# Kernel optimization log

Hardware: AMD Instinct MI355X
Metric: run time of the kernel (lower is better)

Reference implementation:

```python
import jax, jax.numpy as jnp
import numpy as np
from jax import lax

S_DET, S_ANG = 725, 360   # detector bins, projection angles
OUT = 512                 # reconstructed image side
NNZ = 8388608             # nonzeros in sparse backprojection matrix AT
BATCH = 4
BN_EPS = 1e-3             # keras BatchNormalization default epsilon


def _ramp_filter():
    # w_bfunction(pi, linspace(-362, 362, 725))
    s = np.linspace(-np.floor(S_DET / 2), S_DET - np.floor(S_DET / 2) - 1, S_DET)
    v = np.pi * s
    u = np.empty_like(v)
    z = v == 0
    u[z] = 0.5
    nz = ~z
    u[nz] = (np.cos(v[nz]) - 1.0) / v[nz] ** 2 + np.sin(v[nz]) / v[nz]
    return (u * np.pi ** 2 / (4.0 * np.pi ** 2)).astype(np.float32)


def setup_inputs() -> dict:
    key = jax.random.key(0)
    ks = jax.random.split(key, 24)
    p = 0.05
    inp = {
        'inputs': jax.random.normal(ks[0], (BATCH, S_DET, S_ANG, 1), jnp.float32),
        'w_sin1': jax.random.normal(ks[1], (5, 5, 1, 64), jnp.float32) * p,
        'b_sin1': jnp.zeros((64,), jnp.float32),
        'w_sin_mid': jax.random.normal(ks[2], (4, 5, 5, 64, 64), jnp.float32) * p,
        'sin_gamma': jnp.ones((4, 64), jnp.float32),
        'sin_beta': jnp.zeros((4, 64), jnp.float32),
        'sin_mean': jax.random.normal(ks[3], (4, 64), jnp.float32) * 0.1,
        'sin_var': jax.random.uniform(ks[4], (4, 64), jnp.float32, 0.5, 1.5),
        'w_sin6': jax.random.normal(ks[5], (5, 5, 64, 1), jnp.float32) * p,
        'b_sin6': jnp.zeros((1,), jnp.float32),
        'w_ct1': jax.random.normal(ks[6], (5, 5, 1, 64), jnp.float32) * p,
        'b_ct1': jnp.zeros((64,), jnp.float32),
        'w_ct_mid': jax.random.normal(ks[7], (5, 5, 5, 64, 64), jnp.float32) * p,
        'ct_gamma': jnp.ones((5, 64), jnp.float32),
        'ct_beta': jnp.zeros((5, 64), jnp.float32),
        'ct_mean': jax.random.normal(ks[8], (5, 64), jnp.float32) * 0.1,
        'ct_var': jax.random.uniform(ks[9], (5, 64), jnp.float32, 0.5, 1.5),
        'w_ct6': jax.random.normal(ks[10], (5, 5, 64, 1), jnp.float32) * p,
        'b_ct6': jnp.zeros((1,), jnp.float32),
        'w_b': jnp.asarray(_ramp_filter()),
        'at_vals': jax.random.uniform(ks[11], (NNZ,), jnp.float32) * 1e-3,
        'at_rows': jnp.sort(jax.random.randint(ks[12], (NNZ,), 0, OUT * OUT, jnp.int32)),
        'at_cols': jax.random.randint(ks[13], (NNZ,), 0, S_DET * S_ANG, jnp.int32),
    }
    return inp


def _conv2d(x, w, b=None):
    y = lax.conv_general_dilated(x, w, (1, 1), 'SAME',
                                 dimension_numbers=('NHWC', 'HWIO', 'NHWC'))
    return y if b is None else y + b


def _bn(x, g, b, m, v):
    return (x - m) * (g * lax.rsqrt(v + BN_EPS)) + b


def _decode(sin_fan, w_b, at_vals, at_rows, at_cols):
    B = sin_fan.shape[0]
    sf = jnp.transpose(sin_fan, (0, 2, 1, 3))          # [B, 360, 725, 1]
    x = sf.reshape(-1, S_DET, 1)                       # [B*360, 725, 1]
    k = w_b.reshape(S_DET, 1, 1)
    f = lax.conv_general_dilated(x, k, (1,), 'SAME',
                                 dimension_numbers=('NWC', 'WIO', 'NWC'))
    f2 = f.reshape(B, -1).T                            # [261000, B]
    # sparse AT @ f2 via gather + segment_sum
    contrib = at_vals[:, None] * f2[at_cols]           # [nnz, B]
    rf = jax.ops.segment_sum(contrib, at_rows, num_segments=OUT * OUT)
    return 4.0 * rf.T.reshape(B, OUT, OUT, 1)


def reference(inputs, w_sin1, b_sin1, w_sin_mid, sin_gamma, sin_beta, sin_mean,
              sin_var, w_sin6, b_sin6, w_ct1, b_ct1, w_ct_mid, ct_gamma,
              ct_beta, ct_mean, ct_var, w_ct6, b_ct6, w_b, at_vals,
              at_rows, at_cols):
    # --- sinogram domain residual CNN ---
    de = jax.nn.relu(_conv2d(inputs, w_sin1, b_sin1))
    pp = de
    for i in range(4):  # M1 residual blocks
        de = jax.nn.relu(_bn(_conv2d(de, w_sin_mid[i]), sin_gamma[i],
                             sin_beta[i], sin_mean[i], sin_var[i]))
        pp = de + pp
    de_sin = _conv2d(pp / 4.0, w_sin6, b_sin6) + inputs
    # --- filtered backprojection ---
    fbp = _decode(de_sin, w_b, at_vals, at_rows, at_cols)
    # --- image domain residual CNN ---
    out = jax.nn.relu(_conv2d(fbp, w_ct1, b_ct1))
    qq = out
    for i in range(5):  # M2 residual blocks
        out = jax.nn.relu(_bn(_conv2d(out, w_ct_mid[i]), ct_gamma[i],
                              ct_beta[i], ct_mean[i], ct_var[i]))
        qq = qq + out
    outputs = _conv2d(qq / 5.0, w_ct6, b_ct6) + fbp
    return (de_sin, outputs, fbp)
```

## Files before the change

kernel.cpp:

```cpp
#include <hip/hip_runtime.h>
#include <stdint.h>

#define S_DET 725
#define S_ANG 360
#define OUTD  512
#define NB    4

typedef float    float4v __attribute__((ext_vector_type(4)));
typedef int      int4v   __attribute__((ext_vector_type(4)));
typedef _Float16 half8   __attribute__((ext_vector_type(8)));
typedef _Float16 half4   __attribute__((ext_vector_type(4)));
typedef _Float16 half2v  __attribute__((ext_vector_type(2)));

#define GAS __attribute__((address_space(1)))
#define LAS __attribute__((address_space(3)))

__device__ __forceinline__ void async16(const void* src, void* lds) {
  __builtin_amdgcn_global_load_lds((const GAS void*)(uintptr_t)src,
                                   (LAS void*)(uint32_t)(uintptr_t)lds, 16, 0, 0);
}

__global__ __launch_bounds__(256)
void prep_weights(const float* __restrict__ wsin, const float* __restrict__ sg,
                  const float* __restrict__ sb,  const float* __restrict__ sm,
                  const float* __restrict__ sv,
                  const float* __restrict__ wct, const float* __restrict__ cg,
                  const float* __restrict__ cbt, const float* __restrict__ cm,
                  const float* __restrict__ cv,
                  const float* __restrict__ wsin6, const float* __restrict__ wct6,
                  _Float16* __restrict__ wout, float* __restrict__ bout,
                  _Float16* __restrict__ w6out)
{
  int id = blockIdx.x * 256 + threadIdx.x;
  if (id < 9 * 102400) {
    int l   = id / 102400;
    int rem = id - l * 102400;
    int t = rem >> 12;
    int kn = rem & 4095;
    int k = kn >> 6, n = kn & 63;
    const float *w, *g, *b, *m, *v;
    if (l < 4) { w = wsin + l*102400; g = sg + l*64; b = sb + l*64; m = sm + l*64; v = sv + l*64; }
    else { int li = l - 4; w = wct + li*102400; g = cg + li*64; b = cbt + li*64; m = cm + li*64; v = cv + li*64; }
    float s = g[n] * rsqrtf(v[n] + 1e-3f);
    float val = w[rem] * s;
    int slot = (k >> 3) ^ (n & 7);
    wout[(size_t)l*102400 + t*4096 + n*64 + slot*8 + (k & 7)] = (_Float16)val;
    if (rem < 64)
      bout[l*64 + rem] = b[rem] - m[rem] * s;
  } else {
    int r = id - 9 * 102400;
    if (r < 3200)
      w6out[r] = (_Float16)(r < 1600 ? wsin6[r] : wct6[r - 1600]);
  }
}

template <int IMG>
__global__ __launch_bounds__(256)
void conv1_kernel(const float* __restrict__ src, _Float16* __restrict__ dst,
                  const float* __restrict__ w1, const float* __restrict__ b1,
                  int H, int W, int b0)
{
  __shared__ __align__(16) float in_s[400];
  __shared__ __align__(16) float w_s[1600];
  __shared__ float b_s[64];
  const int tid = threadIdx.x;
  const int bz = blockIdx.z, gb = b0 + bz;
  const int y0 = blockIdx.y * 16, x0 = blockIdx.x * 16;
  for (int i = tid; i < 1600; i += 256) w_s[i] = w1[i];
  if (tid < 64) b_s[tid] = b1[tid];
  for (int i = tid; i < 400; i += 256) {
    int iy = i / 20, ix = i - iy * 20;
    int y = y0 - 2 + iy, x = x0 - 2 + ix;
    float v = 0.f;
    if (y >= 0 && y < H && x >= 0 && x < W) {
      if (IMG) v = 4.f * src[(size_t)(y * W + x) * 4 + gb];
      else     v = src[((size_t)gb * H + y) * W + x];
    }
    in_s[i] = v;
  }
  __syncthreads();
  const int ty = tid >> 4, tx = tid & 15;
  float acc[64];
#pragma unroll
  for (int c = 0; c < 64; ++c) acc[c] = 0.f;
  int dy = 0, dx = 0;
  for (int t = 0; t < 25; ++t) {
    float v = in_s[(ty + dy) * 20 + tx + dx];
    const float4v* wp = (const float4v*)(w_s + t * 64);
#pragma unroll
    for (int c = 0; c < 16; ++c) {
      float4v w4 = wp[c];
      acc[4*c+0] += v * w4[0]; acc[4*c+1] += v * w4[1];
      acc[4*c+2] += v * w4[2]; acc[4*c+3] += v * w4[3];
    }
    if (++dx == 5) { dx = 0; ++dy; }
  }
  const int y = y0 + ty, x = x0 + tx;
  if (y < H && x < W) {
    uint32_t* dp = (uint32_t*)(dst + ((size_t)(bz * H + y) * W + x) * 64);
#pragma unroll
    for (int c = 0; c < 32; ++c) {
      float v0 = acc[2*c]   + b_s[2*c];   v0 = v0 > 0.f ? v0 : 0.f;
      float v1 = acc[2*c+1] + b_s[2*c+1]; v1 = v1 > 0.f ? v1 : 0.f;
      half2v h = { (_Float16)v0, (_Float16)v1 };
      dp[c] = __builtin_bit_cast(uint32_t, h);
    }
  }
}

__global__ __launch_bounds__(256, 2)
void mid_conv(const _Float16* __restrict__ src, _Float16* __restrict__ dst,
              float* __restrict__ accum,
              const _Float16* __restrict__ wt, const _Float16* __restrict__ w6g,
              const float* __restrict__ bias, const char* __restrict__ zbuf,
              int H, int W, int b0)
{
  __shared__ __align__(16) char smem[51200 + 2 * 8192 + 3200 + 16];
  char* const atile = smem;
  char* const wbuf  = smem + 51200;
  _Float16* const w6l = (_Float16*)(smem + 51200 + 16384);
  char* const zl = smem + 51200 + 16384 + 3200;
  const int tid = threadIdx.x;
  const int wv = tid >> 6, ln = tid & 63;
  const int bz = blockIdx.z, gb = b0 + bz;
  const int y0 = blockIdx.y * 16, x0 = blockIdx.x * 16;

  if (tid < 200) ((half8*)w6l)[tid] = ((const half8*)w6g)[tid];
  if (tid < 4) ((int*)zl)[tid] = 0;

  for (int inst = wv; inst < 50; inst += 4) {
    const int slot = inst * 64 + ln;
    const int p = slot >> 3, gp = slot & 7;
    const int g = gp ^ (p & 7);
    const int iy = p / 20, ix = p - iy * 20;
    const int y = y0 - 2 + iy, x = x0 - 2 + ix;
    const char* sp = (y >= 0 && y < H && x >= 0 && x < W)
        ? (const char*)(src + ((size_t)(bz * H + y) * W + x) * 64) + g * 16
        : zbuf + g * 16;
    async16(sp, atile + inst * 1024);
  }
#pragma unroll
  for (int j = 0; j < 2; ++j) {
    const int inst = wv * 2 + j;
    async16((const char*)wt + inst * 1024 + ln * 16, wbuf + inst * 1024);
  }
  __syncthreads();

  float4v acc[4][4];
  float4v acc6[4];
#pragma unroll
  for (int pi = 0; pi < 4; ++pi) {
    acc6[pi] = (float4v){0.f, 0.f, 0.f, 0.f};
#pragma unroll
    for (int ci = 0; ci < 4; ++ci) acc[pi][ci] = (float4v){0.f, 0.f, 0.f, 0.f};
  }

  int dy = 0, dx = 0;
  for (int t = 0; t < 25; ++t) {
    if (t < 24) {
      char* wdst = wbuf + ((t + 1) & 1) * 8192;
#pragma unroll
      for (int j = 0; j < 2; ++j) {
        const int inst = wv * 2 + j;
        async16((const char*)wt + (t + 1) * 8192 + inst * 1024 + ln * 16,
                wdst + inst * 1024);
      }
    }
    const char* wb = wbuf + (t & 1) * 8192;
#pragma unroll
    for (int kc = 0; kc < 2; ++kc) {
      const int g0 = kc * 4 + (ln >> 4);
      half8 wf[4], af[4], wf6;
#pragma unroll
      for (int ci = 0; ci < 4; ++ci) {
        const int ch = ci * 16 + (ln & 15);
        wf[ci] = *(const half8*)(wb + ch * 128 + ((g0 ^ (ch & 7)) << 4));
      }
      wf6 = *(const half8*)((ln & 15) == 0
                ? (const char*)(w6l + t * 64 + kc * 32 + ((ln >> 4) << 3))
                : zl);
#pragma unroll
      for (int pi = 0; pi < 4; ++pi) {
        const int p = (wv * 4 + pi + dy) * 20 + (ln & 15) + dx;
        af[pi] = *(const half8*)(atile + p * 128 + ((g0 ^ (p & 7)) << 4));
      }
#pragma unroll
      for (int pi = 0; pi < 4; ++pi) {
#pragma unroll
        for (int ci = 0; ci < 4; ++ci)
          acc[pi][ci] = __builtin_amdgcn_mfma_f32_16x16x32_f16(
              wf[ci], af[pi], acc[pi][ci], 0, 0, 0);
        acc6[pi] = __builtin_amdgcn_mfma_f32_16x16x32_f16(
            wf6, af[pi], acc6[pi], 0, 0, 0);
      }
    }
    if (++dx == 5) { dx = 0; ++dy; }
    __syncthreads();
  }

  const int tx = ln & 15;
  const int x = x0 + tx;
#pragma unroll
  for (int pi = 0; pi < 4; ++pi) {
    const int y = y0 + wv * 4 + pi;
    if (y < H && x < W) {
      _Float16* dp = dst + ((size_t)(bz * H + y) * W + x) * 64;
#pragma unroll
      for (int ci = 0; ci < 4; ++ci) {
        const int cbase = ci * 16 + (ln >> 4) * 4;
        const float4v bv = *(const float4v*)(bias + cbase);
        half4 h;
#pragma unroll
        for (int r = 0; r < 4; ++r) {
          float v = acc[pi][ci][r] + bv[r];
          v = v > 0.f ? v : 0.f;
          h[r] = (_Float16)v;
        }
        *(half4*)(dp + cbase) = h;
      }
    }
  }
  if (ln < 16) {
#pragma unroll
    for (int pi = 0; pi < 4; ++pi) {
      const int y = y0 + wv * 4 + pi, x2 = x0 + ln;
      if (y < H && x2 < W)
        accum[((size_t)gb * H + y) * W + x2] += acc6[pi][0];
    }
  }
}

__global__ __launch_bounds__(256, 2)
void fc_accum(const _Float16* __restrict__ src, float* __restrict__ accum,
              const float* __restrict__ w6, const char* __restrict__ zbuf,
              int H, int W, int b0)
{
  __shared__ __align__(16) char smem[51200 + 3200];
  char* const atile = smem;
  _Float16* const wl = (_Float16*)(smem + 51200);
  const int tid = threadIdx.x;
  const int wv = tid >> 6, ln = tid & 63;
  const int bz = blockIdx.z, gb = b0 + bz;
  const int y0 = blockIdx.y * 16, x0 = blockIdx.x * 16;
  for (int i = tid; i < 1600; i += 256) wl[i] = (_Float16)w6[i];
  for (int inst = wv; inst < 50; inst += 4) {
    const int slot = inst * 64 + ln;
    const int p = slot >> 3, gp = slot & 7;
    const int g = gp ^ (p & 7);
    const int iy = p / 20, ix = p - iy * 20;
    const int y = y0 - 2 + iy, x = x0 - 2 + ix;
    const char* sp = (y >= 0 && y < H && x >= 0 && x < W)
        ? (const char*)(src + ((size_t)(bz * H + y) * W + x) * 64) + g * 16
        : zbuf + g * 16;
    async16(sp, atile + inst * 1024);
  }
  __syncthreads();
  const int ty = tid >> 4, tx = tid & 15;
  float sum = 0.f;
  int dy = 0, dxx = 0;
  for (int t = 0; t < 25; ++t) {
    const int p = (ty + dy) * 20 + tx + dxx;
    const char* pb = atile + p * 128;
    const int pk = p & 7;
    const half2v* wp = (const half2v*)(wl + t * 64);
#pragma unroll
    for (int g = 0; g < 8; ++g) {
      half8 h = *(const half8*)(pb + ((g ^ pk) << 4));
#pragma unroll
      for (int q = 0; q < 4; ++q) {
        half2v a = { h[2*q], h[2*q+1] };
        sum = __builtin_amdgcn_fdot2(a, wp[g * 4 + q], sum, false);
      }
    }
    if (++dxx == 5) { dxx = 0; ++dy; }
  }
  const int y = y0 + ty, x = x0 + tx;
  if (y < H && x < W) accum[((size_t)gb * H + y) * W + x] += sum;
}

__global__ __launch_bounds__(256)
void write_desin(const float* __restrict__ accf, const float* __restrict__ inputs,
                 const float* __restrict__ b6, float* __restrict__ out)
{
  int id = blockIdx.x * 256 + threadIdx.x;
  if (id < NB * S_DET * S_ANG) out[id] = accf[id] * 0.25f + b6[0] + inputs[id];
}

__global__ __launch_bounds__(128)
void ramp_filter(const float* __restrict__ desin, const float* __restrict__ wb,
                 _Float16* __restrict__ f2h)
{
  __shared__ float col[1472];
  __shared__ float wl[725];
  const int blk = blockIdx.x;
  const int b = blk / 360, a = blk - b * 360;
  const int tid = threadIdx.x;
  for (int i = tid; i < 1472; i += 128) col[i] = 0.f;
  for (int i = tid; i < 725; i += 128) wl[i] = wb[i];
  __syncthreads();
  for (int i = tid; i < 725; i += 128) col[368 + i] = desin[(b * 725 + i) * 360 + a];
  __syncthreads();
  const int s0 = tid * 6;
  if (s0 < 725) {
    float o0 = 0, o1 = 0, o2 = 0, o3 = 0, o4 = 0, o5 = 0;
    const float* cb = col + 6 + s0;
    float r0 = cb[0], r1 = cb[1], r2 = cb[2], r3 = cb[3], r4 = cb[4], r5 = cb[5];
    for (int t = 0; t < 725; ++t) {
      float w = wl[t];
      o0 += r0 * w; o1 += r1 * w; o2 += r2 * w;
      o3 += r3 * w; o4 += r4 * w; o5 += r5 * w;
      r0 = r1; r1 = r2; r2 = r3; r3 = r4; r4 = r5; r5 = cb[t + 6];
    }
    float o[6] = { o0, o1, o2, o3, o4, o5 };
#pragma unroll
    for (int j = 0; j < 6; ++j)
      if (s0 + j < 725) f2h[((size_t)a * 725 + s0 + j) * 4 + b] = (_Float16)o[j];
  }
}

__global__ __launch_bounds__(256)
void backproj(const float* __restrict__ vals, const int* __restrict__ rows,
              const int* __restrict__ cols, const _Float16* __restrict__ f2h,
              float* __restrict__ rf)
{
  const int tid = blockIdx.x * 256 + threadIdx.x;
  const int i0 = tid * 16;
  const int4v* rp = (const int4v*)(rows + i0);
  const int4v* cp = (const int4v*)(cols + i0);
  const float4v* vp = (const float4v*)(vals + i0);
  float a0 = 0, a1 = 0, a2 = 0, a3 = 0;
  int4v r0v = __builtin_nontemporal_load(rp);
  int cur = r0v[0];
#pragma unroll
  for (int q = 0; q < 4; ++q) {
    int4v r4 = (q == 0) ? r0v : __builtin_nontemporal_load(rp + q);
    int4v c4 = __builtin_nontemporal_load(cp + q);
    float4v v4 = __builtin_nontemporal_load(vp + q);
#pragma unroll
    for (int u = 0; u < 4; ++u) {
      int r = r4[u]; int c = c4[u]; float v = v4[u];
      if (r != cur) {
        atomicAdd(rf + (size_t)cur * 4 + 0, a0);
        atomicAdd(rf + (size_t)cur * 4 + 1, a1);
        atomicAdd(rf + (size_t)cur * 4 + 2, a2);
        atomicAdd(rf + (size_t)cur * 4 + 3, a3);
        a0 = a1 = a2 = a3 = 0; cur = r;
      }
      const half4 f = *(const half4*)(f2h + (size_t)c * 4);
      a0 += v * (float)f[0]; a1 += v * (float)f[1];
      a2 += v * (float)f[2]; a3 += v * (float)f[3];
    }
  }
  atomicAdd(rf + (size_t)cur * 4 + 0, a0);
  atomicAdd(rf + (size_t)cur * 4 + 1, a1);
  atomicAdd(rf + (size_t)cur * 4 + 2, a2);
  atomicAdd(rf + (size_t)cur * 4 + 3, a3);
}

__global__ __launch_bounds__(256)
void write_fbp(const float* __restrict__ rf, float* __restrict__ out)
{
  int id = blockIdx.x * 256 + threadIdx.x;
  int b = id >> 18, p = id & 262143;
  out[id] = 4.f * rf[(size_t)p * 4 + b];
}

__global__ __launch_bounds__(256)
void write_outputs(const float* __restrict__ accf, const float* __restrict__ rf,
                   const float* __restrict__ b6, float* __restrict__ out)
{
  int id = blockIdx.x * 256 + threadIdx.x;
  int b = id >> 18, p = id & 262143;
  out[id] = accf[id] * 0.2f + b6[0] + 4.f * rf[(size_t)p * 4 + b];
}

extern "C" void kernel_launch(void* const* d_in, const int* in_sizes, int n_in,
                              void* d_out, int out_size, void* d_ws, size_t ws_size,
                              hipStream_t stream)
{
  (void)in_sizes; (void)n_in; (void)out_size;
  const float* inputs   = (const float*)d_in[0];
  const float* w_sin1   = (const float*)d_in[1];
  const float* b_sin1   = (const float*)d_in[2];
  const float* w_sin_mid= (const float*)d_in[3];
  const float* sin_gamma= (const float*)d_in[4];
  const float* sin_beta = (const float*)d_in[5];
  const float* sin_mean = (const float*)d_in[6];
  const float* sin_var  = (const float*)d_in[7];
  const float* w_sin6   = (const float*)d_in[8];
  const float* b_sin6   = (const float*)d_in[9];
  const float* w_ct1    = (const float*)d_in[10];
  const float* b_ct1    = (const float*)d_in[11];
  const float* w_ct_mid = (const float*)d_in[12];
  const float* ct_gamma = (const float*)d_in[13];
  const float* ct_beta  = (const float*)d_in[14];
  const float* ct_mean  = (const float*)d_in[15];
  const float* ct_var   = (const float*)d_in[16];
  const float* w_ct6    = (const float*)d_in[17];
  const float* b_ct6    = (const float*)d_in[18];
  const float* w_b      = (const float*)d_in[19];
  const float* at_vals  = (const float*)d_in[20];
  const int*   at_rows  = (const int*)d_in[21];
  const int*   at_cols  = (const int*)d_in[22];
  float* out = (float*)d_out;

  const size_t base = (size_t)11 << 20;
  const size_t act_per_batch = (size_t)2 * 262144 * 128;
  int nbat = 1;
  if (ws_size >= base + 4 * act_per_batch) nbat = 4;
  else if (ws_size >= base + 2 * act_per_batch) nbat = 2;
  const int npass = 4 / nbat;

  char* ws = (char*)d_ws;
  size_t off = 0;
  auto alloc = [&](size_t bytes) {
    char* p = ws + off;
    off = (off + bytes + 255) & ~(size_t)255;
    return p;
  };
  char*     zbuf    = alloc(256);
  _Float16* wmid    = (_Float16*)alloc((size_t)9 * 102400 * 2);
  float*    biasmid = (float*)alloc(9 * 64 * 4);
  _Float16* w6s     = (_Float16*)alloc(3200 * 2);
  float*    rf      = (float*)alloc((size_t)262144 * 16);
  char*     shreg   = alloc((size_t)262144 * 16);
  _Float16* act_a   = (_Float16*)alloc((size_t)nbat * 262144 * 128);
  _Float16* act_b   = (_Float16*)alloc((size_t)nbat * 262144 * 128);
  _Float16* f2h    = (_Float16*)shreg;
  float*    acc_fc = (float*)shreg;

  hipMemsetAsync(zbuf, 0, 256, stream);
  hipMemsetAsync(rf, 0, (size_t)262144 * 16, stream);
  hipMemsetAsync(acc_fc, 0, (size_t)262144 * 16, stream);

  prep_weights<<<3613, 256, 0, stream>>>(w_sin_mid, sin_gamma, sin_beta, sin_mean, sin_var,
                                         w_ct_mid, ct_gamma, ct_beta, ct_mean, ct_var,
                                         w_sin6, w_ct6, wmid, biasmid, w6s);

  for (int p = 0; p < npass; ++p) {
    const int b0 = p * nbat;
    conv1_kernel<0><<<dim3(23, 46, nbat), 256, 0, stream>>>(inputs, act_a, w_sin1, b_sin1,
                                                            725, 360, b0);
    _Float16* cur = act_a; _Float16* nxt = act_b;
    for (int i = 0; i < 4; ++i) {
      mid_conv<<<dim3(23, 46, nbat), 256, 0, stream>>>(cur, nxt, acc_fc,
                                                       wmid + (size_t)i * 102400, w6s,
                                                       biasmid + i * 64, zbuf, 725, 360, b0);
      _Float16* t = cur; cur = nxt; nxt = t;
    }
    fc_accum<<<dim3(23, 46, nbat), 256, 0, stream>>>(cur, acc_fc, w_sin6, zbuf, 725, 360, b0);
  }
  write_desin<<<4079, 256, 0, stream>>>(acc_fc, inputs, b_sin6, out);

  ramp_filter<<<1440, 128, 0, stream>>>(out, w_b, f2h);
  backproj<<<2048, 256, 0, stream>>>(at_vals, at_rows, at_cols, f2h, rf);
  write_fbp<<<4096, 256, 0, stream>>>(rf, out + 2092576);

  hipMemsetAsync(acc_fc, 0, (size_t)262144 * 16, stream);
  for (int p = 0; p < npass; ++p) {
    const int b0 = p * nbat;
    conv1_kernel<1><<<dim3(32, 32, nbat), 256, 0, stream>>>(rf, act_a, w_ct1, b_ct1,
                                                            512, 512, b0);
    _Float16* cur = act_a; _Float16* nxt = act_b;
    for (int i = 0; i < 5; ++i) {
      mid_conv<<<dim3(32, 32, nbat), 256, 0, stream>>>(cur, nxt, acc_fc,
                                                       wmid + (size_t)(4 + i) * 102400,
                                                       w6s + 1600,
                                                       biasmid + (4 + i) * 64, zbuf,
                                                       512, 512, b0);
      _Float16* t = cur; cur = nxt; nxt = t;
    }
    fc_accum<<<dim3(32, 32, nbat), 256, 0, stream>>>(cur, acc_fc, w_ct6, zbuf, 512, 512, b0);
  }
  write_outputs<<<4096, 256, 0, stream>>>(acc_fc, rf, b_ct6, out + 1044000);
}
```

Baseline: 2.752 ms.

## Move conv1 and final 1-channel conv to MFMA, coarsen backprojection atomics

The first 1-to-64 convolution is rebuilt as an im2col tile in shared memory feeding MFMA, using pre-packed fp16 weights. The final 64-to-1 reduction kernel now uses MFMA with a zero-padded weight fragment, and mid_conv reads that fragment directly from global memory instead of staging it in shared memory. Backprojection threads now handle 64 nonzeros each and use plain stores for rows they fully own, keeping atomics only for the first and last rows. Together these aim to cut scalar FMA work, LDS use and atomic traffic, at the cost of fp16 rounding in conv1 and extra global weight loads.

```diff
diff --git a/kernel.cpp b/kernel.cpp
--- a/kernel.cpp
+++ b/kernel.cpp
@@ -28,8 +28,9 @@
                   const float* __restrict__ cbt, const float* __restrict__ cm,
                   const float* __restrict__ cv,
                   const float* __restrict__ wsin6, const float* __restrict__ wct6,
+                  const float* __restrict__ wsin1, const float* __restrict__ wct1,
                   _Float16* __restrict__ wout, float* __restrict__ bout,
-                  _Float16* __restrict__ w6out)
+                  _Float16* __restrict__ w6out, _Float16* __restrict__ w1fout)
 {
   int id = blockIdx.x * 256 + threadIdx.x;
   if (id < 9 * 102400) {
@@ -49,25 +50,34 @@
       bout[l*64 + rem] = b[rem] - m[rem] * s;
   } else {
     int r = id - 9 * 102400;
-    if (r < 3200)
+    if (r < 3200) {
       w6out[r] = (_Float16)(r < 1600 ? wsin6[r] : wct6[r - 1600]);
+    } else if (r < 3200 + 4096) {
+      int q = r - 3200;
+      int layer = q >> 11;
+      int idx = q & 2047;
+      int ci = idx >> 9, ln = (idx >> 3) & 63, e = idx & 7;
+      int ch = ci * 16 + (ln & 15);
+      int k = (ln >> 4) * 8 + e;
+      float val = 0.f;
+      if (k < 25) val = (layer ? wct1 : wsin1)[k * 64 + ch];
+      w1fout[q] = (_Float16)val;
+    }
   }
 }
 
 template <int IMG>
 __global__ __launch_bounds__(256)
-void conv1_kernel(const float* __restrict__ src, _Float16* __restrict__ dst,
-                  const float* __restrict__ w1, const float* __restrict__ b1,
-                  int H, int W, int b0)
-{
-  __shared__ __align__(16) float in_s[400];
-  __shared__ __align__(16) float w_s[1600];
-  __shared__ float b_s[64];
+void conv1_mfma(const float* __restrict__ src, _Float16* __restrict__ dst,
+                const _Float16* __restrict__ w1f, const float* __restrict__ b1,
+                int H, int W, int b0)
+{
+  __shared__ __align__(16) float rawt[400];
+  __shared__ __align__(16) char imc[256 * 80];
   const int tid = threadIdx.x;
+  const int wv = tid >> 6, ln = tid & 63;
   const int bz = blockIdx.z, gb = b0 + bz;
   const int y0 = blockIdx.y * 16, x0 = blockIdx.x * 16;
-  for (int i = tid; i < 1600; i += 256) w_s[i] = w1[i];
-  if (tid < 64) b_s[tid] = b1[tid];
   for (int i = tid; i < 400; i += 256) {
     int iy = i / 20, ix = i - iy * 20;
     int y = y0 - 2 + iy, x = x0 - 2 + ix;
@@ -76,34 +86,66 @@
       if (IMG) v = 4.f * src[(size_t)(y * W + x) * 4 + gb];
       else     v = src[((size_t)gb * H + y) * W + x];
     }
-    in_s[i] = v;
+    rawt[i] = v;
   }
   __syncthreads();
-  const int ty = tid >> 4, tx = tid & 15;
-  float acc[64];
-#pragma unroll
-  for (int c = 0; c < 64; ++c) acc[c] = 0.f;
-  int dy = 0, dx = 0;
-  for (int t = 0; t < 25; ++t) {
-    float v = in_s[(ty + dy) * 20 + tx + dx];
-    const float4v* wp = (const float4v*)(w_s + t * 64);
-#pragma unroll
-    for (int c = 0; c < 16; ++c) {
-      float4v w4 = wp[c];
-      acc[4*c+0] += v * w4[0]; acc[4*c+1] += v * w4[1];
-      acc[4*c+2] += v * w4[2]; acc[4*c+3] += v * w4[3];
-    }
-    if (++dx == 5) { dx = 0; ++dy; }
-  }
-  const int y = y0 + ty, x = x0 + tx;
-  if (y < H && x < W) {
-    uint32_t* dp = (uint32_t*)(dst + ((size_t)(bz * H + y) * W + x) * 64);
-#pragma unroll
-    for (int c = 0; c < 32; ++c) {
-      float v0 = acc[2*c]   + b_s[2*c];   v0 = v0 > 0.f ? v0 : 0.f;
-      float v1 = acc[2*c+1] + b_s[2*c+1]; v1 = v1 > 0.f ? v1 : 0.f;
-      half2v h = { (_Float16)v0, (_Float16)v1 };
-      dp[c] = __builtin_bit_cast(uint32_t, h);
+  {
+    const int ty = tid >> 4, tx = tid & 15;
+    _Float16 row[32];
+    int dy = 0, dx = 0;
+#pragma unroll
+    for (int t = 0; t < 25; ++t) {
+      row[t] = (_Float16)rawt[(ty + dy) * 20 + tx + dx];
+      if (++dx == 5) { dx = 0; ++dy; }
+    }
+#pragma unroll
+    for (int t = 25; t < 32; ++t) row[t] = (_Float16)0.f;
+    char* dp = imc + tid * 80;
+#pragma unroll
+    for (int j = 0; j < 4; ++j)
+      *(half8*)(dp + j * 16) = *(const half8*)((const char*)row + j * 16);
+  }
+  __syncthreads();
+
+  half8 wf[4];
+#pragma unroll
+  for (int ci = 0; ci < 4; ++ci) wf[ci] = ((const half8*)w1f)[ci * 64 + ln];
+
+  float4v acc[4][4];
+#pragma unroll
+  for (int pi = 0; pi < 4; ++pi)
+#pragma unroll
+    for (int ci = 0; ci < 4; ++ci) acc[pi][ci] = (float4v){0.f, 0.f, 0.f, 0.f};
+
+#pragma unroll
+  for (int pi = 0; pi < 4; ++pi) {
+    const int px = (wv * 4 + pi) * 16 + (ln & 15);
+    half8 af = *(const half8*)(imc + px * 80 + ((ln >> 4) << 4));
+#pragma unroll
+    for (int ci = 0; ci < 4; ++ci)
+      acc[pi][ci] = __builtin_amdgcn_mfma_f32_16x16x32_f16(wf[ci], af, acc[pi][ci], 0, 0, 0);
+  }
+
+  const int tx = ln & 15;
+  const int x = x0 + tx;
+#pragma unroll
+  for (int pi = 0; pi < 4; ++pi) {
+    const int y = y0 + wv * 4 + pi;
+    if (y < H && x < W) {
+      _Float16* dp = dst + ((size_t)(bz * H + y) * W + x) * 64;
+#pragma unroll
+      for (int ci = 0; ci < 4; ++ci) {
+        const int cbase = ci * 16 + (ln >> 4) * 4;
+        const float4v bv = *(const float4v*)(b1 + cbase);
+        half4 h;
+#pragma unroll
+        for (int r = 0; r < 4; ++r) {
+          float v = acc[pi][ci][r] + bv[r];
+          v = v > 0.f ? v : 0.f;
+          h[r] = (_Float16)v;
+        }
+        *(half4*)(dp + cbase) = h;
+      }
     }
   }
 }
@@ -115,18 +157,13 @@
               const float* __restrict__ bias, const char* __restrict__ zbuf,
               int H, int W, int b0)
 {
-  __shared__ __align__(16) char smem[51200 + 2 * 8192 + 3200 + 16];
+  __shared__ __align__(16) char smem[51200 + 2 * 8192];
   char* const atile = smem;
   char* const wbuf  = smem + 51200;
-  _Float16* const w6l = (_Float16*)(smem + 51200 + 16384);
-  char* const zl = smem + 51200 + 16384 + 3200;
   const int tid = threadIdx.x;
   const int wv = tid >> 6, ln = tid & 63;
   const int bz = blockIdx.z, gb = b0 + bz;
   const int y0 = blockIdx.y * 16, x0 = blockIdx.x * 16;
-
-  if (tid < 200) ((half8*)w6l)[tid] = ((const half8*)w6g)[tid];
-  if (tid < 4) ((int*)zl)[tid] = 0;
 
   for (int inst = wv; inst < 50; inst += 4) {
     const int slot = inst * 64 + ln;
@@ -170,15 +207,16 @@
 #pragma unroll
     for (int kc = 0; kc < 2; ++kc) {
       const int g0 = kc * 4 + (ln >> 4);
-      half8 wf[4], af[4], wf6;
+      half8 wf[4], af[4];
+      half8 wf6 = {(_Float16)0, (_Float16)0, (_Float16)0, (_Float16)0,
+                   (_Float16)0, (_Float16)0, (_Float16)0, (_Float16)0};
 #pragma unroll
       for (int ci = 0; ci < 4; ++ci) {
         const int ch = ci * 16 + (ln & 15);
         wf[ci] = *(const half8*)(wb + ch * 128 + ((g0 ^ (ch & 7)) << 4));
       }
-      wf6 = *(const half8*)((ln & 15) == 0
-                ? (const char*)(w6l + t * 64 + kc * 32 + ((ln >> 4) << 3))
-                : zl);
+      if ((ln & 15) == 0)
+        wf6 = *(const half8*)(w6g + t * 64 + kc * 32 + ((ln >> 4) << 3));
 #pragma unroll
       for (int pi = 0; pi < 4; ++pi) {
         const int p = (wv * 4 + pi + dy) * 20 + (ln & 15) + dx;
@@ -230,19 +268,16 @@
   }
 }
 
-__global__ __launch_bounds__(256, 2)
-void fc_accum(const _Float16* __restrict__ src, float* __restrict__ accum,
-              const float* __restrict__ w6, const char* __restrict__ zbuf,
-              int H, int W, int b0)
-{
-  __shared__ __align__(16) char smem[51200 + 3200];
-  char* const atile = smem;
-  _Float16* const wl = (_Float16*)(smem + 51200);
+__global__ __launch_bounds__(256, 3)
+void fc_mfma(const _Float16* __restrict__ src, float* __restrict__ accum,
+             const _Float16* __restrict__ w6g, const char* __restrict__ zbuf,
+             int H, int W, int b0)
+{
+  __shared__ __align__(16) char atile[51200];
   const int tid = threadIdx.x;
   const int wv = tid >> 6, ln = tid & 63;
   const int bz = blockIdx.z, gb = b0 + bz;
   const int y0 = blockIdx.y * 16, x0 = blockIdx.x * 16;
-  for (int i = tid; i < 1600; i += 256) wl[i] = (_Float16)w6[i];
   for (int inst = wv; inst < 50; inst += 4) {
     const int slot = inst * 64 + ln;
     const int p = slot >> 3, gp = slot & 7;
@@ -255,27 +290,37 @@
     async16(sp, atile + inst * 1024);
   }
   __syncthreads();
-  const int ty = tid >> 4, tx = tid & 15;
-  float sum = 0.f;
-  int dy = 0, dxx = 0;
+
+  float4v acc6[4];
+#pragma unroll
+  for (int pi = 0; pi < 4; ++pi) acc6[pi] = (float4v){0.f, 0.f, 0.f, 0.f};
+
+  int dy = 0, dx = 0;
   for (int t = 0; t < 25; ++t) {
-    const int p = (ty + dy) * 20 + tx + dxx;
-    const char* pb = atile + p * 128;
-    const int pk = p & 7;
-    const half2v* wp = (const half2v*)(wl + t * 64);
-#pragma unroll
-    for (int g = 0; g < 8; ++g) {
-      half8 h = *(const half8*)(pb + ((g ^ pk) << 4));
-#pragma unroll
-      for (int q = 0; q < 4; ++q) {
-        half2v a = { h[2*q], h[2*q+1] };
-        sum = __builtin_amdgcn_fdot2(a, wp[g * 4 + q], sum, false);
-      }
-    }
-    if (++dxx == 5) { dxx = 0; ++dy; }
-  }
-  const int y = y0 + ty, x = x0 + tx;
-  if (y < H && x < W) accum[((size_t)gb * H + y) * W + x] += sum;
+#pragma unroll
+    for (int kc = 0; kc < 2; ++kc) {
+      const int g0 = kc * 4 + (ln >> 4);
+      half8 wf6 = {(_Float16)0, (_Float16)0, (_Float16)0, (_Float16)0,
+                   (_Float16)0, (_Float16)0, (_Float16)0, (_Float16)0};
+      if ((ln & 15) == 0)
+        wf6 = *(const half8*)(w6g + t * 64 + kc * 32 + ((ln >> 4) << 3));
+#pragma unroll
+      for (int pi = 0; pi < 4; ++pi) {
+        const int p = (wv * 4 + pi + dy) * 20 + (ln & 15) + dx;
+        half8 af = *(const half8*)(atile + p * 128 + ((g0 ^ (p & 7)) << 4));
+        acc6[pi] = __builtin_amdgcn_mfma_f32_16x16x32_f16(wf6, af, acc6[pi], 0, 0, 0);
+      }
+    }
+    if (++dx == 5) { dx = 0; ++dy; }
+  }
+  if (ln < 16) {
+#pragma unroll
+    for (int pi = 0; pi < 4; ++pi) {
+      const int y = y0 + wv * 4 + pi, x2 = x0 + ln;
+      if (y < H && x2 < W)
+        accum[((size_t)gb * H + y) * W + x2] += acc6[pi][0];
+    }
+  }
 }
 
 __global__ __launch_bounds__(256)
@@ -324,15 +369,16 @@
               float* __restrict__ rf)
 {
   const int tid = blockIdx.x * 256 + threadIdx.x;
-  const int i0 = tid * 16;
+  const size_t i0 = (size_t)tid * 64;
   const int4v* rp = (const int4v*)(rows + i0);
   const int4v* cp = (const int4v*)(cols + i0);
   const float4v* vp = (const float4v*)(vals + i0);
   float a0 = 0, a1 = 0, a2 = 0, a3 = 0;
   int4v r0v = __builtin_nontemporal_load(rp);
   int cur = r0v[0];
-#pragma unroll
-  for (int q = 0; q < 4; ++q) {
+  bool first = true;
+#pragma unroll 4
+  for (int q = 0; q < 16; ++q) {
     int4v r4 = (q == 0) ? r0v : __builtin_nontemporal_load(rp + q);
     int4v c4 = __builtin_nontemporal_load(cp + q);
     float4v v4 = __builtin_nontemporal_load(vp + q);
@@ -340,10 +386,14 @@
     for (int u = 0; u < 4; ++u) {
       int r = r4[u]; int c = c4[u]; float v = v4[u];
       if (r != cur) {
-        atomicAdd(rf + (size_t)cur * 4 + 0, a0);
-        atomicAdd(rf + (size_t)cur * 4 + 1, a1);
-        atomicAdd(rf + (size_t)cur * 4 + 2, a2);
-        atomicAdd(rf + (size_t)cur * 4 + 3, a3);
+        float* p = rf + (size_t)cur * 4;
+        if (first) {
+          atomicAdd(p + 0, a0); atomicAdd(p + 1, a1);
+          atomicAdd(p + 2, a2); atomicAdd(p + 3, a3);
+          first = false;
+        } else {
+          p[0] = a0; p[1] = a1; p[2] = a2; p[3] = a3;
+        }
         a0 = a1 = a2 = a3 = 0; cur = r;
       }
       const half4 f = *(const half4*)(f2h + (size_t)c * 4);
@@ -351,10 +401,9 @@
       a2 += v * (float)f[2]; a3 += v * (float)f[3];
     }
   }
-  atomicAdd(rf + (size_t)cur * 4 + 0, a0);
-  atomicAdd(rf + (size_t)cur * 4 + 1, a1);
-  atomicAdd(rf + (size_t)cur * 4 + 2, a2);
-  atomicAdd(rf + (size_t)cur * 4 + 3, a3);
+  float* p = rf + (size_t)cur * 4;
+  atomicAdd(p + 0, a0); atomicAdd(p + 1, a1);
+  atomicAdd(p + 2, a2); atomicAdd(p + 3, a3);
 }
 
 __global__ __launch_bounds__(256)
@@ -422,6 +471,7 @@
   _Float16* wmid    = (_Float16*)alloc((size_t)9 * 102400 * 2);
   float*    biasmid = (float*)alloc(9 * 64 * 4);
   _Float16* w6s     = (_Float16*)alloc(3200 * 2);
+  _Float16* w1f     = (_Float16*)alloc(4096 * 2);
   float*    rf      = (float*)alloc((size_t)262144 * 16);
   char*     shreg   = alloc((size_t)262144 * 16);
   _Float16* act_a   = (_Float16*)alloc((size_t)nbat * 262144 * 128);
@@ -433,14 +483,15 @@
   hipMemsetAsync(rf, 0, (size_t)262144 * 16, stream);
   hipMemsetAsync(acc_fc, 0, (size_t)262144 * 16, stream);
 
-  prep_weights<<<3613, 256, 0, stream>>>(w_sin_mid, sin_gamma, sin_beta, sin_mean, sin_var,
+  prep_weights<<<3630, 256, 0, stream>>>(w_sin_mid, sin_gamma, sin_beta, sin_mean, sin_var,
                                          w_ct_mid, ct_gamma, ct_beta, ct_mean, ct_var,
-                                         w_sin6, w_ct6, wmid, biasmid, w6s);
+                                         w_sin6, w_ct6, w_sin1, w_ct1,
+                                         wmid, biasmid, w6s, w1f);
 
   for (int p = 0; p < npass; ++p) {
     const int b0 = p * nbat;
-    conv1_kernel<0><<<dim3(23, 46, nbat), 256, 0, stream>>>(inputs, act_a, w_sin1, b_sin1,
-                                                            725, 360, b0);
+    conv1_mfma<0><<<dim3(23, 46, nbat), 256, 0, stream>>>(inputs, act_a, w1f, b_sin1,
+                                                          725, 360, b0);
     _Float16* cur = act_a; _Float16* nxt = act_b;
     for (int i = 0; i < 4; ++i) {
       mid_conv<<<dim3(23, 46, nbat), 256, 0, stream>>>(cur, nxt, acc_fc,
@@ -448,19 +499,19 @@
                                                        biasmid + i * 64, zbuf, 725, 360, b0);
       _Float16* t = cur; cur = nxt; nxt = t;
     }
-    fc_accum<<<dim3(23, 46, nbat), 256, 0, stream>>>(cur, acc_fc, w_sin6, zbuf, 725, 360, b0);
+    fc_mfma<<<dim3(23, 46, nbat), 256, 0, stream>>>(cur, acc_fc, w6s, zbuf, 725, 360, b0);
   }
   write_desin<<<4079, 256, 0, stream>>>(acc_fc, inputs, b_sin6, out);
 
   ramp_filter<<<1440, 128, 0, stream>>>(out, w_b, f2h);
-  backproj<<<2048, 256, 0, stream>>>(at_vals, at_rows, at_cols, f2h, rf);
+  backproj<<<512, 256, 0, stream>>>(at_vals, at_rows, at_cols, f2h, rf);
   write_fbp<<<4096, 256, 0, stream>>>(rf, out + 2092576);
 
   hipMemsetAsync(acc_fc, 0, (size_t)262144 * 16, stream);
   for (int p = 0; p < npass; ++p) {
     const int b0 = p * nbat;
-    conv1_kernel<1><<<dim3(32, 32, nbat), 256, 0, stream>>>(rf, act_a, w_ct1, b_ct1,
-                                                            512, 512, b0);
+    conv1_mfma<1><<<dim3(32, 32, nbat), 256, 0, stream>>>(rf, act_a, w1f + 2048, b_ct1,
+                                                          512, 512, b0);
     _Float16* cur = act_a; _Float16* nxt = act_b;
     for (int i = 0; i < 5; ++i) {
       mid_conv<<<dim3(32, 32, nbat), 256, 0, stream>>>(cur, nxt, acc_fc,
@@ -470,7 +521,8 @@
                                                        512, 512, b0);
       _Float16* t = cur; cur = nxt; nxt = t;
     }
-    fc_accum<<<dim3(32, 32, nbat), 256, 0, stream>>>(cur, acc_fc, w_ct6, zbuf, 512, 512, b0);
+    fc_mfma<<<dim3(32, 32, nbat), 256, 0, stream>>>(cur, acc_fc, w6s + 1600, zbuf,
+                                                    512, 512, b0);
   }
   write_outputs<<<4096, 256, 0, stream>>>(acc_fc, rf, b_ct6, out + 1044000);
 }
```

Result: slower. 2.871 ms (+4.3%).
